# Performance work log

Hardware: AMD Instinct MI355X
Metric: run time of the kernel (lower is better)

## Reference

```python
import jax, jax.numpy as jnp
import numpy as np

DIM = 256
NUM_HEADS = 8
HEAD_DIM = DIM // NUM_HEADS
Z_SHAPE = (32, 32)   # template grid -> qL = 1024
X_SHAPE = (64, 64)   # search grid  -> kvL = 4096
TBL = (max(Z_SHAPE[0], X_SHAPE[0]), max(Z_SHAPE[1], X_SHAPE[1]))  # (64, 64)
N_TABLE = (2 * TBL[0] - 1) * (2 * TBL[1] - 1)  # 16129


def _make_rel_index():
    """Faithful replication of the torch module's buffer construction (numpy, vectorized)."""
    H, W = TBL
    coords = np.stack(np.meshgrid(np.arange(H), np.arange(W), indexing='ij'), 0).reshape(2, -1)
    rel = coords[:, :, None] - coords[:, None, :]                     # (2, HW, HW)
    idx = (rel[0] + H - 1) * (2 * W - 1) + (rel[1] + W - 1)           # (HW, HW)
    h_z_begin = int(H / 2 - Z_SHAPE[0] / 2); h_x_begin = int(H / 2 - X_SHAPE[0] / 2)
    w_z_begin = int(W / 2 - Z_SHAPE[1] / 2); w_x_begin = int(W / 2 - X_SHAPE[1] / 2)
    hz = np.arange(h_z_begin, h_z_begin + Z_SHAPE[0])
    hx = np.arange(h_x_begin, h_x_begin + X_SHAPE[0])
    wz = np.arange(w_z_begin, w_z_begin + Z_SHAPE[1])
    wx = np.arange(w_x_begin, w_x_begin + X_SHAPE[1])
    # NOTE: source multiplies by z_2d_shape[0]/z_2d_shape[1] (kept faithfully, even though it looks odd)
    z_pos = hz[:, None] * Z_SHAPE[0] + wz[None, :]                    # (32, 32) axes (h_z, w_z)
    x_pos = hx[:, None] * Z_SHAPE[1] + wx[None, :]                    # (64, 64) axes (h_x, w_x)
    g = idx[z_pos][:, :, x_pos]                                       # (h_z, w_z, h_x, w_x)
    g = g.transpose(0, 2, 1, 3).reshape(Z_SHAPE[0] * Z_SHAPE[1], X_SHAPE[0] * X_SHAPE[1])
    return jnp.asarray(g, dtype=jnp.int32)                           # (qL, kvL)


def setup_inputs() -> dict:
    key = jax.random.key(0)
    ks = jax.random.split(key, 10)
    B, qL, kvL, C = 4, Z_SHAPE[0] * Z_SHAPE[1], X_SHAPE[0] * X_SHAPE[1], DIM
    return {
        'q': jax.random.normal(ks[0], (B, qL, C), jnp.float32),
        'kv': jax.random.normal(ks[1], (B, kvL, C), jnp.float32),
        'Wq': jax.random.normal(ks[2], (C, C), jnp.float32) * 0.02,
        'bq': jnp.zeros((C,), jnp.float32),
        'Wkv': jax.random.normal(ks[3], (2 * C, C), jnp.float32) * 0.02,
        'bkv': jnp.zeros((2 * C,), jnp.float32),
        'bias_table': jax.random.normal(ks[4], (N_TABLE, NUM_HEADS), jnp.float32) * 0.02,
        'Wp': jax.random.normal(ks[5], (C, C), jnp.float32) * 0.02,
        'bp': jnp.zeros((C,), jnp.float32),
        'rel_index': _make_rel_index(),
    }


def reference(q, kv, Wq, bq, Wkv, bkv, bias_table, Wp, bp, rel_index):
    B, qL, C = q.shape
    kvL = kv.shape[1]
    H, hd = NUM_HEADS, HEAD_DIM
    scale = hd ** (-0.5)
    Q = (q @ Wq.T + bq).reshape(B, qL, H, hd) * scale                  # bqhd
    KV = (kv @ Wkv.T + bkv).reshape(B, kvL, 2, H, hd)
    K, V = KV[:, :, 0], KV[:, :, 1]                                    # bkhd
    attn = jnp.einsum('bqhd,bkhd->bhqk', Q, K)                         # (B,H,qL,kvL)
    bias = bias_table[rel_index]                                       # (qL,kvL,H)
    attn = attn + jnp.transpose(bias, (2, 0, 1))[None]
    attn = jax.nn.softmax(attn, axis=-1)
    x = jnp.einsum('bhqk,bkhd->bqhd', attn, V).reshape(B, qL, C)
    return x @ Wp.T + bp
```

## Files before the change

### kernel.cpp

```cpp
#include <hip/hip_runtime.h>
#include <math.h>

#define DIM 256
#define NUM_HEADS 8
#define HEAD_DIM 32
#define QL 1024
#define KVL 4096
#define BATCH 4
#define NTAB 16129

typedef __attribute__((ext_vector_type(8))) short short8;
typedef __attribute__((ext_vector_type(4))) float floatx4;
typedef __attribute__((ext_vector_type(4))) unsigned short ushort4v;

__device__ inline unsigned short f2bf(float x) {
    unsigned u = __builtin_bit_cast(unsigned, x);
    unsigned r = (u + 0x7FFFu + ((u >> 16) & 1u)) >> 16;
    return (unsigned short)r;
}
__device__ inline float bf2f(unsigned short h) {
    return __builtin_bit_cast(float, (unsigned)h << 16);
}
__device__ inline floatx4 mfma16(short8 a, short8 b, floatx4 c) {
    return __builtin_amdgcn_mfma_f32_16x16x32_bf16(a, b, c, 0, 0, 0);
}

__global__ __launch_bounds__(256) void split_all(
    const float* __restrict__ q, const float* __restrict__ kv,
    const float* __restrict__ Wq, const float* __restrict__ Wkv,
    const float* __restrict__ Wp,
    unsigned short* __restrict__ qh, unsigned short* __restrict__ kvh,
    unsigned short* __restrict__ Wqh, unsigned short* __restrict__ Wkvh,
    unsigned short* __restrict__ Wph, unsigned short* __restrict__ Wpl)
{
    const int gid = blockIdx.x * 256 + threadIdx.x;
    const float* src; unsigned short* dh; unsigned short* dl = nullptr; int local;
    if (gid < 262144)       { src = q;   dh = qh;   local = gid; }
    else if (gid < 1310720) { src = kv;  dh = kvh;  local = gid - 262144; }
    else if (gid < 1327104) { src = Wq;  dh = Wqh;  local = gid - 1310720; }
    else if (gid < 1359872) { src = Wkv; dh = Wkvh; local = gid - 1327104; }
    else                    { src = Wp;  dh = Wph;  dl = Wpl; local = gid - 1359872; }
    const float4 v = ((const float4*)src)[local];
    ushort4v h;
    h[0] = f2bf(v.x); h[1] = f2bf(v.y); h[2] = f2bf(v.z); h[3] = f2bf(v.w);
    ((ushort4v*)dh)[local] = h;
    if (dl) {
        ushort4v l;
        l[0] = f2bf(v.x - bf2f(h[0])); l[1] = f2bf(v.y - bf2f(h[1]));
        l[2] = f2bf(v.z - bf2f(h[2])); l[3] = f2bf(v.w - bf2f(h[3]));
        ((ushort4v*)dl)[local] = l;
    }
}

template<int MODE, int MM, int NN>
__global__ __launch_bounds__(256) void gemm_bf16(
    const unsigned short* __restrict__ Ah, const unsigned short* __restrict__ Al,
    const unsigned short* __restrict__ Wh, const unsigned short* __restrict__ Wl,
    const float* __restrict__ bias, float* __restrict__ Cf,
    unsigned short* __restrict__ Cb, float scale)
{
    constexpr bool THREE = (MODE == 0);
    const int t    = threadIdx.x;
    const int w    = t >> 6;
    const int lane = t & 63;
    const int n16  = lane & 15;
    const int quad = lane >> 4;
    const int m0 = blockIdx.y * 128 + w * 32;
    const int n0 = blockIdx.x * 64;

    floatx4 acc[2][4];
#pragma unroll
    for (int s = 0; s < 2; ++s)
#pragma unroll
        for (int c = 0; c < 4; ++c) acc[s][c] = (floatx4){0.f, 0.f, 0.f, 0.f};

#pragma unroll 2
    for (int kb = 0; kb < 256; kb += 32) {
        short8 af[2], afl[2], wf[4], wfl[4];
#pragma unroll
        for (int s = 0; s < 2; ++s) {
            af[s] = *(const short8*)(Ah + (size_t)(m0 + s * 16 + n16) * 256 + kb + quad * 8);
            if (THREE)
                afl[s] = *(const short8*)(Al + (size_t)(m0 + s * 16 + n16) * 256 + kb + quad * 8);
        }
#pragma unroll
        for (int c = 0; c < 4; ++c) {
            wf[c] = *(const short8*)(Wh + (size_t)(n0 + c * 16 + n16) * 256 + kb + quad * 8);
            if (THREE)
                wfl[c] = *(const short8*)(Wl + (size_t)(n0 + c * 16 + n16) * 256 + kb + quad * 8);
        }
#pragma unroll
        for (int c = 0; c < 4; ++c)
#pragma unroll
            for (int s = 0; s < 2; ++s) {
                acc[s][c] = mfma16(af[s], wf[c], acc[s][c]);
                if (THREE) {
                    acc[s][c] = mfma16(af[s], wfl[c], acc[s][c]);
                    acc[s][c] = mfma16(afl[s], wf[c], acc[s][c]);
                }
            }
    }

#pragma unroll
    for (int s = 0; s < 2; ++s)
#pragma unroll
        for (int c = 0; c < 4; ++c) {
            const floatx4 v = acc[s][c];
            const int n_g = n0 + c * 16 + n16;
#pragma unroll
            for (int r = 0; r < 4; ++r) {
                const int m_g = m0 + s * 16 + quad * 4 + r;
                const float val = v[r];
                if (MODE == 0) {
                    Cf[(size_t)m_g * 256 + n_g] = val + bias[n_g];
                } else if (MODE == 1) {
                    const int h = n_g >> 5, d = n_g & 31;
                    const int b = m_g >> 10, qq = m_g & 1023;
                    Cb[(((size_t)(b * 8 + h) * 1024 + qq) << 5) + d] =
                        f2bf((val + bias[n_g]) * scale);
                } else if (MODE == 2) {
                    const int h = n_g >> 5, d = n_g & 31;
                    const int b = m_g >> 12, kvr = m_g & 4095;
                    Cb[(((size_t)(b * 8 + h) * 4096 + kvr) << 5) + d] =
                        f2bf(val + bias[n_g]);
                } else {
                    const int h = m_g >> 5, dd = m_g & 31;
                    const int b = n_g >> 12, kvr = n_g & 4095;
                    Cb[(((size_t)((b * 8 + h) * 32 + dd)) << 12) + kvr] =
                        f2bf(val + bias[m_g]);
                }
            }
        }
}

__global__ __launch_bounds__(256) void make_bt(
    const float* __restrict__ bias_table, float* __restrict__ Bt)
{
    const int gid = blockIdx.x * 256 + threadIdx.x;
    if (gid < NTAB * 8) {
        const int i = gid >> 3, h = gid & 7;
        Bt[h * NTAB + i] = bias_table[gid];
    }
}

__global__ __launch_bounds__(256, 4) void attn_mfma(
    const unsigned short* __restrict__ Qb,
    const unsigned short* __restrict__ Kb,
    const unsigned short* __restrict__ Vt,
    const float* __restrict__ Bt,
    float* __restrict__ Op,
    float* __restrict__ lp)
{
    const int qt = blockIdx.x;
    const int h  = blockIdx.y;
    const int b  = blockIdx.z >> 2;
    const int sp = blockIdx.z & 3;
    const int bh = b * NUM_HEADS + h;
    const int tid  = threadIdx.x;
    const int w    = tid >> 6;
    const int lane = tid & 63;
    const int n    = lane & 15;
    const int quad = lane >> 4;

    __shared__ __align__(16) unsigned short Ps[4][16 * 72];

    const int qrowA = qt * 64 + w * 16 + n;
    const short8 qf = *(const short8*)(Qb + (((size_t)bh * QL + qrowA) << 5) + quad * 8);

    const int qgC = qt * 64 + w * 16 + quad * 4;
    const float* Bth = Bt + h * NTAB;

    int ivals[4], uvals[4];
#pragma unroll
    for (int r = 0; r < 4; ++r) {
        const int q = qgC + r;
        ivals[r] = q >> 5;
        uvals[r] = q & 31;
    }
    int xjc[4];
#pragma unroll
    for (int c = 0; c < 4; ++c) xjc[c] = c * 16 + n;

    floatx4 o0 = {0.f, 0.f, 0.f, 0.f};
    floatx4 o1 = {0.f, 0.f, 0.f, 0.f};
    float lacc[4] = {0.f, 0.f, 0.f, 0.f};

    const unsigned short* Kbase = Kb + (((size_t)bh * KVL) << 5);
    const unsigned short* Vbase = Vt + (((size_t)bh * 32) << 12);
    const int kbase = sp * 1024;

    for (int kt = 0; kt < 16; ++kt) {
        const int kv0 = kbase + kt * 64;
        const int jS  = (kv0 >> 6) & 31;
        const int vS  = kv0 >> 11;

        short8 kf[4];
#pragma unroll
        for (int c = 0; c < 4; ++c)
            kf[c] = *(const short8*)(Kbase + ((size_t)(kv0 + c * 16 + n) << 5) + quad * 8);
        short8 vf[2][2];
#pragma unroll
        for (int kc = 0; kc < 2; ++kc)
#pragma unroll
            for (int dh = 0; dh < 2; ++dh)
                vf[kc][dh] = *(const short8*)(Vbase + ((size_t)(dh * 16 + n) << 12)
                                              + kv0 + kc * 32 + quad * 8);

        floatx4 sc[4];
#pragma unroll
        for (int c = 0; c < 4; ++c) {
            floatx4 z = {0.f, 0.f, 0.f, 0.f};
            sc[c] = __builtin_amdgcn_mfma_f32_16x16x32_bf16(qf, kf[c], z, 0, 0, 0);
        }

#pragma unroll
        for (int r = 0; r < 4; ++r) {
            const int a  = 528 + (ivals[r] << 5) + jS;
            const int A0 = ((a >> 6) + 63) * 127 + (a & 63) + 63;
            const int B0 = ((uvals[r] << 1) + vS) << 5;
#pragma unroll
            for (int c = 0; c < 4; ++c) {
                const int bb  = B0 + xjc[c];
                const int idx = A0 - ((bb >> 6) * 127 + (bb & 63));
                const float p = __expf(sc[c][r] + Bth[idx]);
                lacc[r] += p;
                Ps[w][(quad * 4 + r) * 72 + c * 16 + n] = f2bf(p);
            }
        }
        asm volatile("s_waitcnt lgkmcnt(0)" ::: "memory");

#pragma unroll
        for (int kc = 0; kc < 2; ++kc) {
            const short8 pf = *(const short8*)(Ps[w] + n * 72 + kc * 32 + quad * 8);
            o0 = __builtin_amdgcn_mfma_f32_16x16x32_bf16(pf, vf[kc][0], o0, 0, 0, 0);
            o1 = __builtin_amdgcn_mfma_f32_16x16x32_bf16(pf, vf[kc][1], o1, 0, 0, 0);
        }
    }

#pragma unroll
    for (int r = 0; r < 4; ++r) {
        float v = lacc[r];
        v += __shfl_xor(v, 1, 16);
        v += __shfl_xor(v, 2, 16);
        v += __shfl_xor(v, 4, 16);
        v += __shfl_xor(v, 8, 16);
        lacc[r] = v;
    }

    float* Opb = Op + (((size_t)(sp * 32 + bh) * QL) << 5);
#pragma unroll
    for (int r = 0; r < 4; ++r) {
        const int qg = qgC + r;
        Opb[((size_t)qg << 5) + n]      = o0[r];
        Opb[((size_t)qg << 5) + 16 + n] = o1[r];
    }
    if (n == 0) {
        float* lpb = lp + (size_t)(sp * 32 + bh) * QL;
#pragma unroll
        for (int r = 0; r < 4; ++r) lpb[qgC + r] = lacc[r];
    }
}

__global__ __launch_bounds__(256) void attn_combine(
    const float* __restrict__ Op, const float* __restrict__ lp,
    unsigned short* __restrict__ Xh, unsigned short* __restrict__ Xl)
{
    const int gid = blockIdx.x * 256 + threadIdx.x;
    const int bhq = gid >> 5, d = gid & 31;
    const int bh = bhq >> 10, q = bhq & 1023;
    const int b = bh >> 3, hh = bh & 7;
    float o = 0.f, l = 0.f;
#pragma unroll
    for (int s = 0; s < 4; ++s) {
        o += Op[((size_t)(s * 32768 + bhq) << 5) + d];
        l += lp[s * 32768 + bhq];
    }
    const float val = o / l;
    const size_t idx = ((size_t)(b * QL + q)) * DIM + hh * HEAD_DIM + d;
    const unsigned short h = f2bf(val);
    Xh[idx] = h;
    Xl[idx] = f2bf(val - bf2f(h));
}

extern "C" void kernel_launch(void* const* d_in, const int* in_sizes, int n_in,
                              void* d_out, int out_size, void* d_ws, size_t ws_size,
                              hipStream_t stream)
{
    const float* q          = (const float*)d_in[0];
    const float* kv         = (const float*)d_in[1];
    const float* Wq         = (const float*)d_in[2];
    const float* bq         = (const float*)d_in[3];
    const float* Wkv        = (const float*)d_in[4];
    const float* bkv        = (const float*)d_in[5];
    const float* bias_table = (const float*)d_in[6];
    const float* Wp         = (const float*)d_in[7];
    const float* bp         = (const float*)d_in[8];
    float* out = (float*)d_out;

    char* ws = (char*)d_ws;
    unsigned short* Qb   = (unsigned short*)(ws);
    unsigned short* Kb   = (unsigned short*)(ws + (size_t)(2u  << 20));
    unsigned short* Vt   = (unsigned short*)(ws + (size_t)(10u << 20));
    unsigned short* kvh  = (unsigned short*)(ws + (size_t)(18u << 20));
    float*          Op   = (float*)         (ws + (size_t)(18u << 20));
    float*          lp   = (float*)         (ws + (size_t)(34u << 20));
    float*          Bt   = (float*)         (ws + (size_t)(34u << 20) + (512u << 10));
    unsigned short* qh   = (unsigned short*)(ws + (size_t)(36u << 20));
    unsigned short* Wqh  = (unsigned short*)(ws + (size_t)(38u << 20));
    unsigned short* Wkvh = (unsigned short*)(ws + (size_t)(38u << 20) + (128u << 10));
    unsigned short* Wph  = (unsigned short*)(ws + (size_t)(38u << 20) + (384u << 10));
    unsigned short* Wpl  = (unsigned short*)(ws + (size_t)(38u << 20) + (512u << 10));
    unsigned short* Xh   = qh;
    unsigned short* Xl   = Vt;

    const float scale = 1.0f / sqrtf((float)HEAD_DIM);

    make_bt<<<dim3((NTAB * 8 + 255) / 256), 256, 0, stream>>>(bias_table, Bt);
    split_all<<<dim3(5376), 256, 0, stream>>>(q, kv, Wq, Wkv, Wp,
                                              qh, kvh, Wqh, Wkvh, Wph, Wpl);
    gemm_bf16<1, 4096, 256><<<dim3(4, 32), 256, 0, stream>>>(
        qh, nullptr, Wqh, nullptr, bq, nullptr, Qb, scale);
    gemm_bf16<2, 16384, 256><<<dim3(4, 128), 256, 0, stream>>>(
        kvh, nullptr, Wkvh, nullptr, bkv, nullptr, Kb, 1.0f);
    gemm_bf16<3, 256, 16384><<<dim3(256, 2), 256, 0, stream>>>(
        Wkvh + 256 * 256, nullptr, kvh, nullptr, bkv + 256, nullptr, Vt, 1.0f);
    attn_mfma<<<dim3(16, 8, 16), 256, 0, stream>>>(Qb, Kb, Vt, Bt, Op, lp);
    attn_combine<<<dim3(4096), 256, 0, stream>>>(Op, lp, Xh, Xl);
    gemm_bf16<0, 4096, 256><<<dim3(4, 32), 256, 0, stream>>>(
        Xh, Xl, Wph, Wpl, bp, out, nullptr, 1.0f);
}
```

Baseline: 260.7 us.

## Fuse bias-table transpose, double-buffer GEMM and attention loads, precompute bias indices

Folds the bias-table transpose into the split kernel and pre-scales it by log2(e), so softmax numerators can use exp2 with an FMA. The GEMM and attention kernels now double-buffer register loads, prefetching the next K tile while the current one computes. Per-lane bias index offsets are hoisted out of the attention loop, and bias values are loaded before the score MFMAs. Block size for the small GEMMs is halved to launch more blocks, and attention occupancy hint drops from 4 to 3, trading occupancy for extra registers.

```diff
diff --git a/kernel.cpp b/kernel.cpp
--- a/kernel.cpp
+++ b/kernel.cpp
@@ -8,6 +8,7 @@
 #define KVL 4096
 #define BATCH 4
 #define NTAB 16129
+#define LOG2E 1.4426950408889634f
 
 typedef __attribute__((ext_vector_type(8))) short short8;
 typedef __attribute__((ext_vector_type(4))) float floatx4;
@@ -28,12 +29,26 @@
 __global__ __launch_bounds__(256) void split_all(
     const float* __restrict__ q, const float* __restrict__ kv,
     const float* __restrict__ Wq, const float* __restrict__ Wkv,
-    const float* __restrict__ Wp,
+    const float* __restrict__ Wp, const float* __restrict__ bias_table,
     unsigned short* __restrict__ qh, unsigned short* __restrict__ kvh,
     unsigned short* __restrict__ Wqh, unsigned short* __restrict__ Wkvh,
-    unsigned short* __restrict__ Wph, unsigned short* __restrict__ Wpl)
+    unsigned short* __restrict__ Wph, unsigned short* __restrict__ Wpl,
+    float* __restrict__ Bt)
 {
     const int gid = blockIdx.x * 256 + threadIdx.x;
+    if (gid >= 1408514) return;
+    if (gid >= 1376256) {
+        const int local = gid - 1376256;
+        const float4 v = ((const float4*)bias_table)[local];
+        const float vv[4] = {v.x, v.y, v.z, v.w};
+        const int base = local * 4;
+#pragma unroll
+        for (int j = 0; j < 4; ++j) {
+            const int i = (base + j) >> 3, h = (base + j) & 7;
+            Bt[h * NTAB + i] = vv[j] * LOG2E;
+        }
+        return;
+    }
     const float* src; unsigned short* dh; unsigned short* dl = nullptr; int local;
     if (gid < 262144)       { src = q;   dh = qh;   local = gid; }
     else if (gid < 1310720) { src = kv;  dh = kvh;  local = gid - 262144; }
@@ -52,8 +67,8 @@
     }
 }
 
-template<int MODE, int MM, int NN>
-__global__ __launch_bounds__(256) void gemm_bf16(
+template<int MODE, int BW>
+__global__ __launch_bounds__(BW * 64) void gemm_bf16(
     const unsigned short* __restrict__ Ah, const unsigned short* __restrict__ Al,
     const unsigned short* __restrict__ Wh, const unsigned short* __restrict__ Wl,
     const float* __restrict__ bias, float* __restrict__ Cf,
@@ -65,7 +80,7 @@
     const int lane = t & 63;
     const int n16  = lane & 15;
     const int quad = lane >> 4;
-    const int m0 = blockIdx.y * 128 + w * 32;
+    const int m0 = blockIdx.y * (BW * 32) + w * 32;
     const int n0 = blockIdx.x * 64;
 
     floatx4 acc[2][4];
@@ -74,29 +89,36 @@
 #pragma unroll
         for (int c = 0; c < 4; ++c) acc[s][c] = (floatx4){0.f, 0.f, 0.f, 0.f};
 
-#pragma unroll 2
-    for (int kb = 0; kb < 256; kb += 32) {
-        short8 af[2], afl[2], wf[4], wfl[4];
+    short8 af[2][2], afl[2][2], wf[2][4], wfl[2][4];
+
+    auto LD = [&](int kb, int bi) {
 #pragma unroll
         for (int s = 0; s < 2; ++s) {
-            af[s] = *(const short8*)(Ah + (size_t)(m0 + s * 16 + n16) * 256 + kb + quad * 8);
+            af[bi][s] = *(const short8*)(Ah + (size_t)(m0 + s * 16 + n16) * 256 + kb + quad * 8);
             if (THREE)
-                afl[s] = *(const short8*)(Al + (size_t)(m0 + s * 16 + n16) * 256 + kb + quad * 8);
+                afl[bi][s] = *(const short8*)(Al + (size_t)(m0 + s * 16 + n16) * 256 + kb + quad * 8);
         }
 #pragma unroll
         for (int c = 0; c < 4; ++c) {
-            wf[c] = *(const short8*)(Wh + (size_t)(n0 + c * 16 + n16) * 256 + kb + quad * 8);
+            wf[bi][c] = *(const short8*)(Wh + (size_t)(n0 + c * 16 + n16) * 256 + kb + quad * 8);
             if (THREE)
-                wfl[c] = *(const short8*)(Wl + (size_t)(n0 + c * 16 + n16) * 256 + kb + quad * 8);
-        }
+                wfl[bi][c] = *(const short8*)(Wl + (size_t)(n0 + c * 16 + n16) * 256 + kb + quad * 8);
+        }
+    };
+
+    LD(0, 0);
+#pragma unroll
+    for (int i = 0; i < 8; ++i) {
+        const int cur = i & 1, nxt = cur ^ 1;
+        if (i < 7) LD((i + 1) * 32, nxt);
 #pragma unroll
         for (int c = 0; c < 4; ++c)
 #pragma unroll
             for (int s = 0; s < 2; ++s) {
-                acc[s][c] = mfma16(af[s], wf[c], acc[s][c]);
+                acc[s][c] = mfma16(af[cur][s], wf[cur][c], acc[s][c]);
                 if (THREE) {
-                    acc[s][c] = mfma16(af[s], wfl[c], acc[s][c]);
-                    acc[s][c] = mfma16(afl[s], wf[c], acc[s][c]);
+                    acc[s][c] = mfma16(af[cur][s], wfl[cur][c], acc[s][c]);
+                    acc[s][c] = mfma16(afl[cur][s], wf[cur][c], acc[s][c]);
                 }
             }
     }
@@ -133,17 +155,7 @@
         }
 }
 
-__global__ __launch_bounds__(256) void make_bt(
-    const float* __restrict__ bias_table, float* __restrict__ Bt)
-{
-    const int gid = blockIdx.x * 256 + threadIdx.x;
-    if (gid < NTAB * 8) {
-        const int i = gid >> 3, h = gid & 7;
-        Bt[h * NTAB + i] = bias_table[gid];
-    }
-}
-
-__global__ __launch_bounds__(256, 4) void attn_mfma(
+__global__ __launch_bounds__(256, 3) void attn_mfma(
     const unsigned short* __restrict__ Qb,
     const unsigned short* __restrict__ Kb,
     const unsigned short* __restrict__ Vt,
@@ -170,16 +182,20 @@
     const int qgC = qt * 64 + w * 16 + quad * 4;
     const float* Bth = Bt + h * NTAB;
 
-    int ivals[4], uvals[4];
+    const int vS = sp >> 1;
+    int ivals[4];
+    int M[4][4];
 #pragma unroll
     for (int r = 0; r < 4; ++r) {
         const int q = qgC + r;
         ivals[r] = q >> 5;
-        uvals[r] = q & 31;
-    }
-    int xjc[4];
-#pragma unroll
-    for (int c = 0; c < 4; ++c) xjc[c] = c * 16 + n;
+        const int B0 = (((q & 31) << 1) + vS) << 5;
+#pragma unroll
+        for (int c = 0; c < 4; ++c) {
+            const int bb = B0 + c * 16 + n;
+            M[r][c] = (bb >> 6) * 127 + (bb & 63);
+        }
+    }
 
     floatx4 o0 = {0.f, 0.f, 0.f, 0.f};
     floatx4 o1 = {0.f, 0.f, 0.f, 0.f};
@@ -189,15 +205,32 @@
     const unsigned short* Vbase = Vt + (((size_t)bh * 32) << 12);
     const int kbase = sp * 1024;
 
+    short8 kf[2][4];
+    auto LDK = [&](int kt, int bi) {
+        const int kv0 = kbase + kt * 64;
+#pragma unroll
+        for (int c = 0; c < 4; ++c)
+            kf[bi][c] = *(const short8*)(Kbase + ((size_t)(kv0 + c * 16 + n) << 5) + quad * 8);
+    };
+
+    LDK(0, 0);
+
+#pragma unroll
     for (int kt = 0; kt < 16; ++kt) {
+        const int cur = kt & 1, nxt = cur ^ 1;
         const int kv0 = kbase + kt * 64;
-        const int jS  = (kv0 >> 6) & 31;
-        const int vS  = kv0 >> 11;
-
-        short8 kf[4];
-#pragma unroll
-        for (int c = 0; c < 4; ++c)
-            kf[c] = *(const short8*)(Kbase + ((size_t)(kv0 + c * 16 + n) << 5) + quad * 8);
+
+        const int jS = ((sp << 4) + kt) & 31;
+        float bv[16];
+#pragma unroll
+        for (int r = 0; r < 4; ++r) {
+            const int a  = 528 + (ivals[r] << 5) + jS;
+            const int A0 = ((a >> 6) + 63) * 127 + (a & 63) + 63;
+#pragma unroll
+            for (int c = 0; c < 4; ++c)
+                bv[r * 4 + c] = Bth[A0 - M[r][c]];
+        }
+
         short8 vf[2][2];
 #pragma unroll
         for (int kc = 0; kc < 2; ++kc)
@@ -206,35 +239,32 @@
                 vf[kc][dh] = *(const short8*)(Vbase + ((size_t)(dh * 16 + n) << 12)
                                               + kv0 + kc * 32 + quad * 8);
 
+        if (kt < 15) LDK(kt + 1, nxt);
+
         floatx4 sc[4];
 #pragma unroll
         for (int c = 0; c < 4; ++c) {
             floatx4 z = {0.f, 0.f, 0.f, 0.f};
-            sc[c] = __builtin_amdgcn_mfma_f32_16x16x32_bf16(qf, kf[c], z, 0, 0, 0);
-        }
-
-#pragma unroll
-        for (int r = 0; r < 4; ++r) {
-            const int a  = 528 + (ivals[r] << 5) + jS;
-            const int A0 = ((a >> 6) + 63) * 127 + (a & 63) + 63;
-            const int B0 = ((uvals[r] << 1) + vS) << 5;
+            sc[c] = mfma16(qf, kf[cur][c], z);
+        }
+
+#pragma unroll
+        for (int r = 0; r < 4; ++r)
 #pragma unroll
             for (int c = 0; c < 4; ++c) {
-                const int bb  = B0 + xjc[c];
-                const int idx = A0 - ((bb >> 6) * 127 + (bb & 63));
-                const float p = __expf(sc[c][r] + Bth[idx]);
+                const float p = exp2f(fmaf(sc[c][r], LOG2E, bv[r * 4 + c]));
                 lacc[r] += p;
                 Ps[w][(quad * 4 + r) * 72 + c * 16 + n] = f2bf(p);
             }
-        }
         asm volatile("s_waitcnt lgkmcnt(0)" ::: "memory");
 
 #pragma unroll
         for (int kc = 0; kc < 2; ++kc) {
             const short8 pf = *(const short8*)(Ps[w] + n * 72 + kc * 32 + quad * 8);
-            o0 = __builtin_amdgcn_mfma_f32_16x16x32_bf16(pf, vf[kc][0], o0, 0, 0, 0);
-            o1 = __builtin_amdgcn_mfma_f32_16x16x32_bf16(pf, vf[kc][1], o1, 0, 0, 0);
-        }
+            o0 = mfma16(pf, vf[kc][0], o0);
+            o1 = mfma16(pf, vf[kc][1], o1);
+        }
+        asm volatile("" ::: "memory");
     }
 
 #pragma unroll
@@ -315,17 +345,16 @@
 
     const float scale = 1.0f / sqrtf((float)HEAD_DIM);
 
-    make_bt<<<dim3((NTAB * 8 + 255) / 256), 256, 0, stream>>>(bias_table, Bt);
-    split_all<<<dim3(5376), 256, 0, stream>>>(q, kv, Wq, Wkv, Wp,
-                                              qh, kvh, Wqh, Wkvh, Wph, Wpl);
-    gemm_bf16<1, 4096, 256><<<dim3(4, 32), 256, 0, stream>>>(
+    split_all<<<dim3(5503), 256, 0, stream>>>(q, kv, Wq, Wkv, Wp, bias_table,
+                                              qh, kvh, Wqh, Wkvh, Wph, Wpl, Bt);
+    gemm_bf16<1, 2><<<dim3(4, 64), 128, 0, stream>>>(
         qh, nullptr, Wqh, nullptr, bq, nullptr, Qb, scale);
-    gemm_bf16<2, 16384, 256><<<dim3(4, 128), 256, 0, stream>>>(
+    gemm_bf16<2, 4><<<dim3(4, 128), 256, 0, stream>>>(
         kvh, nullptr, Wkvh, nullptr, bkv, nullptr, Kb, 1.0f);
-    gemm_bf16<3, 256, 16384><<<dim3(256, 2), 256, 0, stream>>>(
+    gemm_bf16<3, 4><<<dim3(256, 2), 256, 0, stream>>>(
         Wkvh + 256 * 256, nullptr, kvh, nullptr, bkv + 256, nullptr, Vt, 1.0f);
     attn_mfma<<<dim3(16, 8, 16), 256, 0, stream>>>(Qb, Kb, Vt, Bt, Op, lp);
     attn_combine<<<dim3(4096), 256, 0, stream>>>(Op, lp, Xh, Xl);
-    gemm_bf16<0, 4096, 256><<<dim3(4, 32), 256, 0, stream>>>(
+    gemm_bf16<0, 2><<<dim3(4, 64), 128, 0, stream>>>(
         Xh, Xl, Wph, Wpl, bp, out, nullptr, 1.0f);
 }
```

New measurement: 249.2 us. 4.4% less time.
